# Kernel optimization log

Measured on AMD Instinct MI355X. Metric: run time of the kernel, lower is better.

## Reference

```python
import jax, jax.numpy as jnp
import numpy as np

EPS = 1e-7
MAX_NORM = 1.0 - 1e-3  # projection radius of the unit Poincare ball (c=1)
ALPHA = 0.2            # LeakyReLU negative slope
NEG_INF = -9e15


def _proj(x, max_norm=MAX_NORM):
    # Project points back inside the Poincare ball along the last dim.
    norm = jnp.clip(jnp.linalg.norm(x, axis=-1, keepdims=True), EPS)
    return jnp.where(norm > max_norm, x / norm * max_norm, x)


def _logmap0(x):
    # Log map at the origin of the Poincare ball, c = 1.
    norm = jnp.clip(jnp.linalg.norm(x, axis=-1, keepdims=True), EPS, 1.0 - EPS)
    return jnp.arctanh(norm) * x / norm


def _expmap0(v):
    # Exp map at the origin of the Poincare ball, c = 1.
    norm = jnp.clip(jnp.linalg.norm(v, axis=-1, keepdims=True), EPS)
    return jnp.tanh(norm) * v / norm


def setup_inputs() -> dict:
    key = jax.random.key(0)
    k1, k2, k3 = jax.random.split(key, 3)
    N, D = 12288, 128
    # points strictly inside the ball: ||x|| ~ 0.01*sqrt(128) ~ 0.11 < 1
    x = jax.random.normal(k1, (N, D), dtype=jnp.float32) * 0.01
    adj = jax.random.randint(k2, (N, N), 0, 2, dtype=jnp.int32)
    # attention vector a, as in init: N(0, 0.2) then proj(a, 0.9) row-wise
    a = jax.random.normal(k3, (2 * D, 1), dtype=jnp.float32) * 0.2
    a = _proj(a, 0.9)
    return {"x": x, "adj": adj, "a": a}


def reference(x, adj, a):
    D = a.shape[0] // 2
    x_tan = _logmap0(x)                       # [N, D]
    wh1 = x_tan @ a[:D]                       # [N, 1]
    wh2 = x_tan @ a[D:]                       # [N, 1]
    e = jax.nn.leaky_relu(wh1 + wh2.T, ALPHA)  # [N, N] additive scores
    scores = jnp.where(adj > 0, e, NEG_INF)
    attention = jax.nn.softmax(scores, axis=1)  # dropout omitted (eval mode)
    x_tan_prime = attention @ x_tan            # [N, D]
    return _proj(_expmap0(x_tan_prime))
```

## Files before the change

### kernel.cpp

```cpp
#include <hip/hip_runtime.h>
#include <math.h>

#define NN 12288
#define DD 128
#define EPSF 1e-7f
#define MAXNORM (1.0f - 1e-3f)
#define S_SLABS 24

typedef __attribute__((ext_vector_type(8))) short short8_t;
typedef __attribute__((ext_vector_type(4))) float float4_t;
typedef unsigned short ushort_t;

__device__ __forceinline__ unsigned short f2bf(float f) {
    unsigned int u = __builtin_bit_cast(unsigned int, f);
    unsigned int r = u + 0x7FFFu + ((u >> 16) & 1u);
    return (unsigned short)(r >> 16);
}

__global__ __launch_bounds__(128) void prep_kernel(
    const float* __restrict__ x, const float* __restrict__ a,
    ushort_t* __restrict__ xtb,
    float* __restrict__ wh1, float* __restrict__ wh2)
{
    const int r = blockIdx.x;
    const int t = threadIdx.x;
    const float xv = x[r * DD + t];
    const float a1 = a[t];
    const float a2 = a[DD + t];
    float s0 = xv * xv, s1 = xv * a1, s2 = xv * a2;
    #pragma unroll
    for (int o = 32; o > 0; o >>= 1) {
        s0 += __shfl_xor(s0, o);
        s1 += __shfl_xor(s1, o);
        s2 += __shfl_xor(s2, o);
    }
    __shared__ float red[6];
    const int w = t >> 6;
    if ((t & 63) == 0) { red[w * 3 + 0] = s0; red[w * 3 + 1] = s1; red[w * 3 + 2] = s2; }
    __syncthreads();
    const float sumsq = red[0] + red[3];
    const float d1    = red[1] + red[4];
    const float d2    = red[2] + red[5];
    const float nraw  = sqrtf(sumsq);
    const float nrm   = fminf(fmaxf(nraw, EPSF), 1.0f - EPSF);
    const float scale = atanhf(nrm) / nrm;
    xtb[(size_t)r * DD + t] = f2bf(xv * scale);
    if (t == 0) {
        wh1[r] = scale * d1;
        wh2[r] = scale * d2;
    }
}

__global__ __launch_bounds__(256) void swizzle_kernel(
    const ushort_t* __restrict__ xtb, ushort_t* __restrict__ xtB)
{
    __shared__ ushort_t raw[32 * 136];
    const int C = blockIdx.x;
    const int t = threadIdx.x;
    #pragma unroll
    for (int p = 0; p < 2; ++p) {
        const int idx = p * 256 + t;
        const int j = idx >> 4, cell = idx & 15;
        const uint4 v = *(const uint4*)(xtb + (size_t)(C * 32 + j) * DD + cell * 8);
        *(uint4*)&raw[j * 136 + cell * 8] = v;
    }
    __syncthreads();
    #pragma unroll
    for (int p = 0; p < 2; ++p) {
        const int oc = p * 256 + t;
        const int dt = oc >> 6;
        const int l6 = oc & 63;
        const int l15 = l6 & 15, q = l6 >> 4;
        short8_t v;
        #pragma unroll
        for (int e = 0; e < 8; ++e)
            v[e] = (short)raw[(q * 8 + e) * 136 + dt * 16 + l15];
        *(short8_t*)(xtB + (size_t)C * 4096 + oc * 8) = v;
    }
}

__global__ __launch_bounds__(256, 1) void attn_kernel(
    const int* __restrict__ adj,
    const ushort_t* __restrict__ xtB,
    const float* __restrict__ wh1, const float* __restrict__ wh2,
    float* __restrict__ pout, float* __restrict__ plsum)
{
    __shared__ __align__(16) ushort_t B_lds[512 * DD];
    __shared__ __align__(16) float wh2_lds[512];

    const int t = threadIdx.x;
    const int w = t >> 6, lane = t & 63;
    const int l15 = lane & 15, quad = lane >> 4;
    const int s = blockIdx.y;
    const int jcol0 = s * 512;
    const int rowbase = blockIdx.x * 256 + w * 64;

    {
        const uint4* src = (const uint4*)(xtB + (size_t)(jcol0 >> 5) * 4096);
        uint4* dst = (uint4*)B_lds;
        #pragma unroll
        for (int m = 0; m < 32; ++m) dst[m * 256 + t] = src[m * 256 + t];
        wh2_lds[t]       = wh2[jcol0 + t];
        wh2_lds[256 + t] = wh2[jcol0 + 256 + t];
    }

    float wh1r[4];
    #pragma unroll
    for (int it = 0; it < 4; ++it) wh1r[it] = wh1[rowbase + it * 16 + l15];

    __syncthreads();

    const int* adj_lane = adj + (size_t)(rowbase + l15) * NN + jcol0 + quad * 8;

    float4_t acc[8];
    float lsum = 0.0f;
    int4 A0[8], A1[8], A2[8];

    auto load_step = [&](int st, int4 (&A)[8]) {
        const int it = st >> 2, jh = st & 3;
        const int* bp = adj_lane + (size_t)it * 16 * NN + jh * 128;
        #pragma unroll
        for (int kc = 0; kc < 4; ++kc) {
            A[kc * 2 + 0] = *(const int4*)(bp + kc * 32);
            A[kc * 2 + 1] = *(const int4*)(bp + kc * 32 + 4);
        }
    };

    auto process = [&](int st, int4 (&A)[8]) {
        const int it = st >> 2, jh = st & 3;
        if (jh == 0) {
            #pragma unroll
            for (int dt = 0; dt < 8; ++dt) acc[dt] = (float4_t)0.0f;
            lsum = 0.0f;
        }
        const float wh1i = wh1r[it];
        #pragma unroll
        for (int kc = 0; kc < 4; ++kc) {
            const int wbase = jh * 128 + kc * 32 + quad * 8;
            const float4 Wa = *(const float4*)&wh2_lds[wbase];
            const float4 Wb = *(const float4*)&wh2_lds[wbase + 4];
            const int4 Aa = A[kc * 2 + 0], Ac = A[kc * 2 + 1];
            const float u0 = wh1i + Wa.x, u1 = wh1i + Wa.y;
            const float u2 = wh1i + Wa.z, u3 = wh1i + Wa.w;
            const float u4 = wh1i + Wb.x, u5 = wh1i + Wb.y;
            const float u6 = wh1i + Wb.z, u7 = wh1i + Wb.w;
            const float p0 = (Aa.x > 0) ? __expf(fmaxf(u0, 0.2f * u0)) : 0.0f;
            const float p1 = (Aa.y > 0) ? __expf(fmaxf(u1, 0.2f * u1)) : 0.0f;
            const float p2 = (Aa.z > 0) ? __expf(fmaxf(u2, 0.2f * u2)) : 0.0f;
            const float p3 = (Aa.w > 0) ? __expf(fmaxf(u3, 0.2f * u3)) : 0.0f;
            const float p4 = (Ac.x > 0) ? __expf(fmaxf(u4, 0.2f * u4)) : 0.0f;
            const float p5 = (Ac.y > 0) ? __expf(fmaxf(u5, 0.2f * u5)) : 0.0f;
            const float p6 = (Ac.z > 0) ? __expf(fmaxf(u6, 0.2f * u6)) : 0.0f;
            const float p7 = (Ac.w > 0) ? __expf(fmaxf(u7, 0.2f * u7)) : 0.0f;
            lsum += ((p0 + p1) + (p2 + p3)) + ((p4 + p5) + (p6 + p7));
            short8_t af;
            af[0] = (short)f2bf(p0); af[1] = (short)f2bf(p1);
            af[2] = (short)f2bf(p2); af[3] = (short)f2bf(p3);
            af[4] = (short)f2bf(p4); af[5] = (short)f2bf(p5);
            af[6] = (short)f2bf(p6); af[7] = (short)f2bf(p7);
            const int cb = (jh * 4 + kc) * 4096;
            #pragma unroll
            for (int dt = 0; dt < 8; ++dt) {
                const short8_t Bf = *(const short8_t*)&B_lds[cb + dt * 512 + lane * 8];
                acc[dt] = __builtin_amdgcn_mfma_f32_16x16x32_bf16(af, Bf, acc[dt], 0, 0, 0);
            }
        }
        if (jh == 3) {
            float v = lsum;
            v += __shfl_xor(v, 16);
            v += __shfl_xor(v, 32);
            const int row0 = rowbase + it * 16;
            if (quad == 0) plsum[(size_t)s * NN + row0 + l15] = v;
            #pragma unroll
            for (int dt = 0; dt < 8; ++dt)
                #pragma unroll
                for (int reg = 0; reg < 4; ++reg)
                    pout[((size_t)s * NN + row0 + quad * 4 + reg) * DD + dt * 16 + l15]
                        = acc[dt][reg];
        }
    };

    load_step(0, A0);
    load_step(1, A1);
    #pragma unroll
    for (int st = 0; st < 16; ++st) {
        if (st + 2 < 16) {
            const int m2 = (st + 2) % 3;
            if (m2 == 0)      load_step(st + 2, A0);
            else if (m2 == 1) load_step(st + 2, A1);
            else              load_step(st + 2, A2);
        }
        const int m = st % 3;
        if (m == 0)      process(st, A0);
        else if (m == 1) process(st, A1);
        else             process(st, A2);
    }
}

__global__ __launch_bounds__(128) void reduce_kernel(
    const float* __restrict__ pout, const float* __restrict__ plsum,
    float* __restrict__ out)
{
    const int i = blockIdx.x;
    const int t = threadIdx.x;
    float v = 0.0f;
    for (int s = 0; s < S_SLABS; ++s) v += pout[((size_t)s * NN + i) * DD + t];
    float ls = 0.0f;
    for (int s = 0; s < S_SLABS; ++s) ls += plsum[(size_t)s * NN + i];
    v /= ls;
    float ss = v * v;
    #pragma unroll
    for (int o = 1; o < 64; o <<= 1) ss += __shfl_xor(ss, o);
    __shared__ float r2[2];
    if ((t & 63) == 0) r2[t >> 6] = ss;
    __syncthreads();
    const float total = r2[0] + r2[1];
    const float nraw = sqrtf(total);
    const float nv   = fmaxf(nraw, EPSF);
    const float th   = tanhf(nv);
    const float ysc  = th / nv;
    const float nyr  = ysc * nraw;
    const float ny   = fmaxf(nyr, EPSF);
    const float psc  = (ny > MAXNORM) ? (MAXNORM / ny) : 1.0f;
    const float os   = ysc * psc;
    out[(size_t)i * DD + t] = v * os;
}

extern "C" void kernel_launch(void* const* d_in, const int* in_sizes, int n_in,
                              void* d_out, int out_size, void* d_ws, size_t ws_size,
                              hipStream_t stream) {
    const float* x   = (const float*)d_in[0];
    const int*   adj = (const int*)d_in[1];
    const float* a   = (const float*)d_in[2];
    float* out = (float*)d_out;

    char* ws = (char*)d_ws;
    ushort_t* xtb = (ushort_t*)ws;  ws += (size_t)NN * DD * sizeof(ushort_t);
    ushort_t* xtB = (ushort_t*)ws;  ws += (size_t)NN * DD * sizeof(ushort_t);
    float* wh1 = (float*)ws;        ws += NN * sizeof(float);
    float* wh2 = (float*)ws;        ws += NN * sizeof(float);
    float* plsum = (float*)ws;      ws += (size_t)S_SLABS * NN * sizeof(float);
    float* pout  = (float*)ws;

    prep_kernel<<<NN, 128, 0, stream>>>(x, a, xtb, wh1, wh2);
    swizzle_kernel<<<NN / 32, 256, 0, stream>>>(xtb, xtB);
    attn_kernel<<<dim3(NN / 256, S_SLABS), 256, 0, stream>>>(
        adj, xtB, wh1, wh2, pout, plsum);
    reduce_kernel<<<NN, 128, 0, stream>>>(pout, plsum, out);
}
```

Measured before the change: 858.8 us.

## Stream B operand from global memory and split columns into four long chunks

```diff
diff --git a/kernel.cpp b/kernel.cpp
--- a/kernel.cpp
+++ b/kernel.cpp
@@ -5,7 +5,9 @@
 #define DD 128
 #define EPSF 1e-7f
 #define MAXNORM (1.0f - 1e-3f)
-#define S_SLABS 24
+#define CSPLIT 4
+#define CCOLS (NN / CSPLIT)
+#define CSTEPS (CCOLS / 128)
 
 typedef __attribute__((ext_vector_type(8))) short short8_t;
 typedef __attribute__((ext_vector_type(4))) float float4_t;
@@ -79,46 +81,38 @@
     }
 }
 
-__global__ __launch_bounds__(256, 1) void attn_kernel(
+__global__ __launch_bounds__(256, 2) void attn_kernel(
     const int* __restrict__ adj,
     const ushort_t* __restrict__ xtB,
     const float* __restrict__ wh1, const float* __restrict__ wh2,
     float* __restrict__ pout, float* __restrict__ plsum)
 {
-    __shared__ __align__(16) ushort_t B_lds[512 * DD];
-    __shared__ __align__(16) float wh2_lds[512];
+    __shared__ __align__(16) float wh2_lds[CCOLS];
 
     const int t = threadIdx.x;
     const int w = t >> 6, lane = t & 63;
     const int l15 = lane & 15, quad = lane >> 4;
-    const int s = blockIdx.y;
-    const int jcol0 = s * 512;
-    const int rowbase = blockIdx.x * 256 + w * 64;
-
-    {
-        const uint4* src = (const uint4*)(xtB + (size_t)(jcol0 >> 5) * 4096);
-        uint4* dst = (uint4*)B_lds;
-        #pragma unroll
-        for (int m = 0; m < 32; ++m) dst[m * 256 + t] = src[m * 256 + t];
-        wh2_lds[t]       = wh2[jcol0 + t];
-        wh2_lds[256 + t] = wh2[jcol0 + 256 + t];
-    }
-
-    float wh1r[4];
-    #pragma unroll
-    for (int it = 0; it < 4; ++it) wh1r[it] = wh1[rowbase + it * 16 + l15];
-
+    const int cy = blockIdx.y;
+    const int jcol0 = cy * CCOLS;
+    const int rowbase = blockIdx.x * 64 + w * 16;
+
+    #pragma unroll
+    for (int m = 0; m < CCOLS / 256; ++m)
+        wh2_lds[m * 256 + t] = wh2[jcol0 + m * 256 + t];
+    const float wh1i = wh1[rowbase + l15];
     __syncthreads();
 
     const int* adj_lane = adj + (size_t)(rowbase + l15) * NN + jcol0 + quad * 8;
+    const ushort_t* Bbase = xtB + (size_t)(jcol0 >> 5) * 4096 + (size_t)lane * 8;
 
     float4_t acc[8];
+    #pragma unroll
+    for (int dt = 0; dt < 8; ++dt) acc[dt] = (float4_t)0.0f;
     float lsum = 0.0f;
     int4 A0[8], A1[8], A2[8];
 
     auto load_step = [&](int st, int4 (&A)[8]) {
-        const int it = st >> 2, jh = st & 3;
-        const int* bp = adj_lane + (size_t)it * 16 * NN + jh * 128;
+        const int* bp = adj_lane + st * 128;
         #pragma unroll
         for (int kc = 0; kc < 4; ++kc) {
             A[kc * 2 + 0] = *(const int4*)(bp + kc * 32);
@@ -127,16 +121,9 @@
     };
 
     auto process = [&](int st, int4 (&A)[8]) {
-        const int it = st >> 2, jh = st & 3;
-        if (jh == 0) {
-            #pragma unroll
-            for (int dt = 0; dt < 8; ++dt) acc[dt] = (float4_t)0.0f;
-            lsum = 0.0f;
-        }
-        const float wh1i = wh1r[it];
         #pragma unroll
         for (int kc = 0; kc < 4; ++kc) {
-            const int wbase = jh * 128 + kc * 32 + quad * 8;
+            const int wbase = st * 128 + kc * 32 + quad * 8;
             const float4 Wa = *(const float4*)&wh2_lds[wbase];
             const float4 Wb = *(const float4*)&wh2_lds[wbase + 4];
             const int4 Aa = A[kc * 2 + 0], Ac = A[kc * 2 + 1];
@@ -158,33 +145,20 @@
             af[2] = (short)f2bf(p2); af[3] = (short)f2bf(p3);
             af[4] = (short)f2bf(p4); af[5] = (short)f2bf(p5);
             af[6] = (short)f2bf(p6); af[7] = (short)f2bf(p7);
-            const int cb = (jh * 4 + kc) * 4096;
+            const ushort_t* Bp = Bbase + (size_t)(st * 4 + kc) * 4096;
             #pragma unroll
             for (int dt = 0; dt < 8; ++dt) {
-                const short8_t Bf = *(const short8_t*)&B_lds[cb + dt * 512 + lane * 8];
+                const short8_t Bf = *(const short8_t*)(Bp + dt * 512);
                 acc[dt] = __builtin_amdgcn_mfma_f32_16x16x32_bf16(af, Bf, acc[dt], 0, 0, 0);
             }
         }
-        if (jh == 3) {
-            float v = lsum;
-            v += __shfl_xor(v, 16);
-            v += __shfl_xor(v, 32);
-            const int row0 = rowbase + it * 16;
-            if (quad == 0) plsum[(size_t)s * NN + row0 + l15] = v;
-            #pragma unroll
-            for (int dt = 0; dt < 8; ++dt)
-                #pragma unroll
-                for (int reg = 0; reg < 4; ++reg)
-                    pout[((size_t)s * NN + row0 + quad * 4 + reg) * DD + dt * 16 + l15]
-                        = acc[dt][reg];
-        }
     };
 
     load_step(0, A0);
     load_step(1, A1);
     #pragma unroll
-    for (int st = 0; st < 16; ++st) {
-        if (st + 2 < 16) {
+    for (int st = 0; st < CSTEPS; ++st) {
+        if (st + 2 < CSTEPS) {
             const int m2 = (st + 2) % 3;
             if (m2 == 0)      load_step(st + 2, A0);
             else if (m2 == 1) load_step(st + 2, A1);
@@ -195,6 +169,17 @@
         else if (m == 1) process(st, A1);
         else             process(st, A2);
     }
+
+    float v = lsum;
+    v += __shfl_xor(v, 16);
+    v += __shfl_xor(v, 32);
+    if (quad == 0) plsum[(size_t)cy * NN + rowbase + l15] = v;
+    #pragma unroll
+    for (int dt = 0; dt < 8; ++dt)
+        #pragma unroll
+        for (int reg = 0; reg < 4; ++reg)
+            pout[((size_t)cy * NN + rowbase + quad * 4 + reg) * DD + dt * 16 + l15]
+                = acc[dt][reg];
 }
 
 __global__ __launch_bounds__(128) void reduce_kernel(
@@ -204,9 +189,11 @@
     const int i = blockIdx.x;
     const int t = threadIdx.x;
     float v = 0.0f;
-    for (int s = 0; s < S_SLABS; ++s) v += pout[((size_t)s * NN + i) * DD + t];
+    #pragma unroll
+    for (int s = 0; s < CSPLIT; ++s) v += pout[((size_t)s * NN + i) * DD + t];
     float ls = 0.0f;
-    for (int s = 0; s < S_SLABS; ++s) ls += plsum[(size_t)s * NN + i];
+    #pragma unroll
+    for (int s = 0; s < CSPLIT; ++s) ls += plsum[(size_t)s * NN + i];
     v /= ls;
     float ss = v * v;
     #pragma unroll
@@ -239,12 +226,12 @@
     ushort_t* xtB = (ushort_t*)ws;  ws += (size_t)NN * DD * sizeof(ushort_t);
     float* wh1 = (float*)ws;        ws += NN * sizeof(float);
     float* wh2 = (float*)ws;        ws += NN * sizeof(float);
-    float* plsum = (float*)ws;      ws += (size_t)S_SLABS * NN * sizeof(float);
+    float* plsum = (float*)ws;      ws += (size_t)CSPLIT * NN * sizeof(float);
     float* pout  = (float*)ws;
 
     prep_kernel<<<NN, 128, 0, stream>>>(x, a, xtb, wh1, wh2);
     swizzle_kernel<<<NN / 32, 256, 0, stream>>>(xtb, xtB);
-    attn_kernel<<<dim3(NN / 256, S_SLABS), 256, 0, stream>>>(
+    attn_kernel<<<dim3(NN / 64, CSPLIT), 256, 0, stream>>>(
         adj, xtB, wh1, wh2, pout, plsum);
     reduce_kernel<<<NN, 128, 0, stream>>>(pout, plsum, out);
 }
```

Result: slower. 1.719 ms (+100.2%).
